# Optimization experiments

Hardware: AMD Instinct MI355X
Metric: run time of the kernel (lower is better)

## Reference

```python
import jax, jax.numpy as jnp
import numpy as np

N_NODES = 50000
N_EDGES = 800000
N_ENTS = 200000
N_RELS = 500
D = 128


def setup_inputs() -> dict:
    key = jax.random.key(0)
    ks = jax.random.split(key, 9)
    return {
        "prev_ent_embs": jax.random.normal(ks[0], (N_ENTS, D), dtype=jnp.float32),
        "rel_embs": jax.random.normal(ks[1], (N_RELS, D), dtype=jnp.float32),
        "loop_weight": jax.random.normal(ks[2], (D, D), dtype=jnp.float32) * 0.1,
        "evolve_loop_weight": jax.random.normal(ks[3], (D, D), dtype=jnp.float32) * 0.1,
        "weight_neighbor": jax.random.normal(ks[4], (D, D), dtype=jnp.float32) * 0.1,
        "node_id": jax.random.randint(ks[5], (N_NODES,), 0, N_ENTS, dtype=jnp.int64) if jax.config.jax_enable_x64 else jax.random.randint(ks[5], (N_NODES,), 0, N_ENTS, dtype=jnp.int32),
        "src": jax.random.randint(ks[6], (N_EDGES,), 0, N_NODES, dtype=jnp.int32),
        "dst": jax.random.randint(ks[7], (N_EDGES,), 0, N_NODES, dtype=jnp.int32),
        "etype": jax.random.randint(ks[8], (N_EDGES,), 0, N_RELS, dtype=jnp.int32),
    }


def reference(prev_ent_embs, rel_embs, loop_weight, evolve_loop_weight,
              weight_neighbor, node_id, src, dst, etype):
    n_nodes = node_id.shape[0]
    # node features gathered from global entity table
    h = prev_ent_embs[node_id]                                    # [N, D]

    # per-edge message: (h[src] + rel[type]) @ W_neighbor
    msg = (h[src] + rel_embs[etype]) @ weight_neighbor            # [E, D]

    # scatter-sum into destination nodes
    agg = jax.ops.segment_sum(msg, dst, num_segments=n_nodes)     # [N, D]

    # in-degree and norm (apply_func: h * in_norm, standard 1/in_degree)
    deg = jax.ops.segment_sum(jnp.ones_like(dst, dtype=h.dtype), dst,
                              num_segments=n_nodes)               # [N]
    has_in = deg > 0
    in_norm = jnp.where(has_in, 1.0 / jnp.maximum(deg, 1.0), 0.0)[:, None]
    agg = agg * in_norm

    # self-loop: loop_weight where in_degree>0, evolve_loop_weight otherwise
    loop_msg = jnp.where(has_in[:, None], h @ loop_weight, h @ evolve_loop_weight)

    # activation (dropout=0 -> identity in eval)
    return jax.nn.relu(agg + loop_msg)
```

## Files before the change

kernel.cpp:

```cpp
#include <hip/hip_runtime.h>
#include <hip/hip_bf16.h>
#include <stdint.h>

#define N_NODES 50000
#define N_EDGES 800000
#define N_ENTS  200000
#define N_RELS  500
#define DIM     128

#define DEGS 32
#define CAP  64

#define ZERO_REC ((int)(50000u | (500u << 16)))

using f32x4  = __attribute__((ext_vector_type(4))) float;
using bf16x8 = __attribute__((ext_vector_type(8))) short;

static __device__ __forceinline__ ushort f_to_bf16(float f) {
    __hip_bfloat16 h = __float2bfloat16(f);
    return *reinterpret_cast<ushort*>(&h);
}
static __device__ __forceinline__ uint pack2(float a, float b) {
    return (uint)f_to_bf16(a) | ((uint)f_to_bf16(b) << 16);
}
static __device__ __forceinline__ float blo(uint u) { return __uint_as_float(u << 16); }
static __device__ __forceinline__ float bhi(uint u) { return __uint_as_float(u & 0xffff0000u); }

__global__ __launch_bounds__(256) void k_front(
        const float* __restrict__ prev, const int* __restrict__ node_id,
        ushort* __restrict__ afull,
        const int* __restrict__ dst, const int* __restrict__ src,
        const int* __restrict__ etype,
        int* __restrict__ deg, uint* __restrict__ srcpk,
        const float* __restrict__ rel, ushort* __restrict__ rel_bf,
        const float* __restrict__ Wn, const float* __restrict__ Wl,
        ushort* __restrict__ WfT) {
    int blk = blockIdx.x;
    if (blk < 3125) {
        int e = blk * 256 + threadIdx.x;
        if (e < N_EDGES) {
            int dn = dst[e];
            uint rec = (uint)src[e] | ((uint)etype[e] << 16);
            int r = atomicAdd(&deg[dn * DEGS], 1);
            if (r < CAP) srcpk[dn * CAP + r] = rec;
        }
    } else if (blk < 6250) {
        int i = (blk - 3125) * 256 + threadIdx.x;
        int row = i >> 4, c = (i & 15) * 8;
        int nid = node_id[row];
        const float* p = prev + (size_t)nid * DIM + c;
        float4 v0 = *(const float4*)p;
        float4 v1 = *(const float4*)(p + 4);
        uint4 w;
        w.x = pack2(v0.x, v0.y);
        w.y = pack2(v0.z, v0.w);
        w.z = pack2(v1.x, v1.y);
        w.w = pack2(v1.z, v1.w);
        *(uint4*)(afull + (size_t)row * 256 + 128 + c) = w;
    } else if (blk < 6504) {
        int i = (blk - 6250) * 256 + threadIdx.x;
        if (i < 128 * 256) {
            int n = i >> 8, k = i & 255;
            float v = (k < 128) ? Wn[k * 128 + n] : Wl[(k - 128) * 128 + n];
            WfT[i] = f_to_bf16(v);
        } else {
            int j = i - 128 * 256;
            if (j < N_RELS * 64) {
                float2 v = *(const float2*)(rel + j * 2);
                *(uint*)(rel_bf + j * 2) = pack2(v.x, v.y);
            }
        }
    } else {
        int t = threadIdx.x;
        if (t < 128)       ((uint*)(afull + (size_t)50000 * 256))[t] = 0u;
        else if (t < 192)  ((uint*)(rel_bf + 500 * 128))[t - 128]    = 0u;
    }
}

__global__ __launch_bounds__(256) void k_agg(ushort* __restrict__ afull,
                                             const ushort* __restrict__ rel_bf,
                                             const uint* __restrict__ srcpk,
                                             const int* __restrict__ deg) {
    int wave = threadIdx.x >> 6, lane = threadIdx.x & 63;
    int n = blockIdx.x * 4 + wave;
    if (n >= N_NODES) return;
    int d = deg[n * DEGS];
    int cnt = min(d, CAP);
    int g = lane >> 4, q = lane & 15;
    const ushort* hb = afull + 128 + q * 8;
    const ushort* rb = rel_bf + q * 8;
    float acc[8] = {0.f, 0.f, 0.f, 0.f, 0.f, 0.f, 0.f, 0.f};

#define ACC4(hv, rv)                                              \
    acc[0] += blo(hv.x) + blo(rv.x); acc[1] += bhi(hv.x) + bhi(rv.x); \
    acc[2] += blo(hv.y) + blo(rv.y); acc[3] += bhi(hv.y) + bhi(rv.y); \
    acc[4] += blo(hv.z) + blo(rv.z); acc[5] += bhi(hv.z) + bhi(rv.z); \
    acc[6] += blo(hv.w) + blo(rv.w); acc[7] += bhi(hv.w) + bhi(rv.w);

    int rec = (lane < cnt) ? (int)srcpk[n * CAP + lane] : ZERO_REC;
    for (int j = 0; j < cnt; j += 8) {
        uint e0 = (uint)__shfl(rec, j + g);
        uint e1 = (uint)__shfl(rec, j + 4 + g);
        uint4 h0 = *(const uint4*)(hb + (size_t)(e0 & 0xffffu) * 256);
        uint4 r0 = *(const uint4*)(rb + (e0 >> 16) * 128);
        uint4 h1 = *(const uint4*)(hb + (size_t)(e1 & 0xffffu) * 256);
        uint4 r1 = *(const uint4*)(rb + (e1 >> 16) * 128);
        ACC4(h0, r0);
        ACC4(h1, r1);
    }
#undef ACC4

#pragma unroll
    for (int i = 0; i < 8; i++) {
        acc[i] += __shfl_xor(acc[i], 16);
        acc[i] += __shfl_xor(acc[i], 32);
    }
    float norm = (d > 0) ? 1.0f / (float)d : 0.0f;
    if (g == 0) {
        uint4 w;
        w.x = pack2(acc[0] * norm, acc[1] * norm);
        w.y = pack2(acc[2] * norm, acc[3] * norm);
        w.z = pack2(acc[4] * norm, acc[5] * norm);
        w.w = pack2(acc[6] * norm, acc[7] * norm);
        *(uint4*)(afull + (size_t)n * 256 + q * 8) = w;
    }
}

#define LDSK 264
__global__ __launch_bounds__(256) void k_mm(const ushort* __restrict__ afull,
                                            const ushort* __restrict__ WfT,
                                            float* __restrict__ out) {
    __shared__ ushort wl[128 * LDSK];
    for (int idx = threadIdx.x; idx < 128 * 32; idx += 256) {
        int n = idx >> 5, p = idx & 31;
        uint4 v = *(const uint4*)(WfT + n * 256 + p * 8);
        *(uint4*)(&wl[n * LDSK + p * 8]) = v;
    }
    __syncthreads();

    int wave = threadIdx.x >> 6, lane = threadIdx.x & 63;
    int m = lane & 15, quad = lane >> 4;
    int rowBase = blockIdx.x * 128 + wave * 32;

    f32x4 acc[2][8];
#pragma unroll
    for (int rt = 0; rt < 2; rt++)
#pragma unroll
        for (int ct = 0; ct < 8; ct++) acc[rt][ct] = f32x4{0.f, 0.f, 0.f, 0.f};

    int r0 = rowBase + m;      if (r0 > N_NODES - 1) r0 = N_NODES - 1;
    int r1 = rowBase + 16 + m; if (r1 > N_NODES - 1) r1 = N_NODES - 1;
    const ushort* pa0 = afull + (size_t)r0 * 256 + quad * 8;
    const ushort* pa1 = afull + (size_t)r1 * 256 + quad * 8;

#pragma unroll
    for (int ks = 0; ks < 8; ks++) {
        bf16x8 a0 = *(const bf16x8*)(pa0 + ks * 32);
        bf16x8 a1 = *(const bf16x8*)(pa1 + ks * 32);
#pragma unroll
        for (int ct = 0; ct < 8; ct++) {
            bf16x8 b = *(const bf16x8*)(&wl[(ct * 16 + m) * LDSK + ks * 32 + quad * 8]);
            acc[0][ct] = __builtin_amdgcn_mfma_f32_16x16x32_bf16(a0, b, acc[0][ct], 0, 0, 0);
            acc[1][ct] = __builtin_amdgcn_mfma_f32_16x16x32_bf16(a1, b, acc[1][ct], 0, 0, 0);
        }
    }

#pragma unroll
    for (int rt = 0; rt < 2; rt++) {
        int rbase = rowBase + rt * 16 + quad * 4;
#pragma unroll
        for (int reg = 0; reg < 4; reg++) {
            int grow = rbase + reg;
            if (grow < N_NODES) {
#pragma unroll
                for (int ct = 0; ct < 8; ct++) {
                    float v = acc[rt][ct][reg];
                    out[(size_t)grow * 128 + ct * 16 + m] = v > 0.f ? v : 0.f;
                }
            }
        }
    }
}

__global__ __launch_bounds__(256) void k_fixup(const ushort* __restrict__ afull,
                                               const float* __restrict__ We,
                                               const int* __restrict__ deg,
                                               float* __restrict__ out) {
    int n = blockIdx.x * 256 + threadIdx.x;
    if (n >= N_NODES) return;
    if (deg[n * DEGS] != 0) return;
    for (int c = 0; c < 128; c++) {
        float a = 0.f;
        for (int k = 0; k < 128; k++) {
            float h = blo((uint)afull[(size_t)n * 256 + 128 + k]);
            a += h * We[k * 128 + c];
        }
        out[(size_t)n * 128 + c] = a > 0.f ? a : 0.f;
    }
}

extern "C" void kernel_launch(void* const* d_in, const int* in_sizes, int n_in,
                              void* d_out, int out_size, void* d_ws, size_t ws_size,
                              hipStream_t stream) {
    const float* prev  = (const float*)d_in[0];
    const float* rel   = (const float*)d_in[1];
    const float* Wl    = (const float*)d_in[2];
    const float* We    = (const float*)d_in[3];
    const float* Wn    = (const float*)d_in[4];
    const int* node_id = (const int*)d_in[5];
    const int* src     = (const int*)d_in[6];
    const int* dst     = (const int*)d_in[7];
    const int* etype   = (const int*)d_in[8];
    float* out = (float*)d_out;

    char* ws = (char*)d_ws;
    ushort* afull  = (ushort*)(ws);
    ushort* WfT    = (ushort*)(ws + 25600512);
    ushort* rel_bf = (ushort*)(ws + 25666048);
    int* deg       = (int*)(ws + 25794304);
    uint* srcpk    = (uint*)(ws + 32194304);

    hipMemsetAsync(deg, 0, 6400000, stream);
    k_front <<<6505,  256, 0, stream>>>(prev, node_id, afull, dst, src, etype,
                                        deg, srcpk, rel, rel_bf, Wn, Wl, WfT);
    k_agg   <<<12500, 256, 0, stream>>>(afull, rel_bf, srcpk, deg);
    k_mm    <<<391,   256, 0, stream>>>(afull, WfT, out);
    k_fixup <<<196,   256, 0, stream>>>(afull, We, deg, out);
}
```

Baseline: 243.3 us.

## Vectorize edge bucketing, unroll aggregation gathers, fold zero-degree fixup into GEMM

Each thread in the edge-bucketing phase now handles four edges, loaded as int4 vectors, which cuts the front kernel's block count. The aggregation loop gathers 16 edges per iteration instead of 8 to keep more loads in flight. The separate fixup kernel for zero in-degree nodes is removed. Its scalar evolve-weight matmul now runs inside the GEMM epilogue behind a rarely taken branch, saving one launch at the cost of possible divergence inside the MFMA kernel.

New measurement: 270.0 us. 11.0% more time.

```diff
diff --git a/kernel.cpp b/kernel.cpp
--- a/kernel.cpp
+++ b/kernel.cpp
@@ -36,16 +36,25 @@
         const float* __restrict__ Wn, const float* __restrict__ Wl,
         ushort* __restrict__ WfT) {
     int blk = blockIdx.x;
-    if (blk < 3125) {
-        int e = blk * 256 + threadIdx.x;
+    if (blk < 782) {
+        int t = blk * 256 + threadIdx.x;
+        int e = t * 4;
         if (e < N_EDGES) {
-            int dn = dst[e];
-            uint rec = (uint)src[e] | ((uint)etype[e] << 16);
-            int r = atomicAdd(&deg[dn * DEGS], 1);
-            if (r < CAP) srcpk[dn * CAP + r] = rec;
-        }
-    } else if (blk < 6250) {
-        int i = (blk - 3125) * 256 + threadIdx.x;
+            int4 d4 = *(const int4*)(dst + e);
+            int4 s4 = *(const int4*)(src + e);
+            int4 t4 = *(const int4*)(etype + e);
+            int r;
+            r = atomicAdd(&deg[d4.x * DEGS], 1);
+            if (r < CAP) srcpk[d4.x * CAP + r] = (uint)s4.x | ((uint)t4.x << 16);
+            r = atomicAdd(&deg[d4.y * DEGS], 1);
+            if (r < CAP) srcpk[d4.y * CAP + r] = (uint)s4.y | ((uint)t4.y << 16);
+            r = atomicAdd(&deg[d4.z * DEGS], 1);
+            if (r < CAP) srcpk[d4.z * CAP + r] = (uint)s4.z | ((uint)t4.z << 16);
+            r = atomicAdd(&deg[d4.w * DEGS], 1);
+            if (r < CAP) srcpk[d4.w * CAP + r] = (uint)s4.w | ((uint)t4.w << 16);
+        }
+    } else if (blk < 3907) {
+        int i = (blk - 782) * 256 + threadIdx.x;
         int row = i >> 4, c = (i & 15) * 8;
         int nid = node_id[row];
         const float* p = prev + (size_t)nid * DIM + c;
@@ -57,8 +66,8 @@
         w.z = pack2(v1.x, v1.y);
         w.w = pack2(v1.z, v1.w);
         *(uint4*)(afull + (size_t)row * 256 + 128 + c) = w;
-    } else if (blk < 6504) {
-        int i = (blk - 6250) * 256 + threadIdx.x;
+    } else if (blk < 4161) {
+        int i = (blk - 3907) * 256 + threadIdx.x;
         if (i < 128 * 256) {
             int n = i >> 8, k = i & 255;
             float v = (k < 128) ? Wn[k * 128 + n] : Wl[(k - 128) * 128 + n];
@@ -98,15 +107,23 @@
     acc[6] += blo(hv.w) + blo(rv.w); acc[7] += bhi(hv.w) + bhi(rv.w);
 
     int rec = (lane < cnt) ? (int)srcpk[n * CAP + lane] : ZERO_REC;
-    for (int j = 0; j < cnt; j += 8) {
+    for (int j = 0; j < cnt; j += 16) {
         uint e0 = (uint)__shfl(rec, j + g);
         uint e1 = (uint)__shfl(rec, j + 4 + g);
+        uint e2 = (uint)__shfl(rec, j + 8 + g);
+        uint e3 = (uint)__shfl(rec, j + 12 + g);
         uint4 h0 = *(const uint4*)(hb + (size_t)(e0 & 0xffffu) * 256);
         uint4 r0 = *(const uint4*)(rb + (e0 >> 16) * 128);
         uint4 h1 = *(const uint4*)(hb + (size_t)(e1 & 0xffffu) * 256);
         uint4 r1 = *(const uint4*)(rb + (e1 >> 16) * 128);
+        uint4 h2 = *(const uint4*)(hb + (size_t)(e2 & 0xffffu) * 256);
+        uint4 r2 = *(const uint4*)(rb + (e2 >> 16) * 128);
+        uint4 h3 = *(const uint4*)(hb + (size_t)(e3 & 0xffffu) * 256);
+        uint4 r3 = *(const uint4*)(rb + (e3 >> 16) * 128);
         ACC4(h0, r0);
         ACC4(h1, r1);
+        ACC4(h2, r2);
+        ACC4(h3, r3);
     }
 #undef ACC4
 
@@ -129,6 +146,8 @@
 #define LDSK 264
 __global__ __launch_bounds__(256) void k_mm(const ushort* __restrict__ afull,
                                             const ushort* __restrict__ WfT,
+                                            const int* __restrict__ deg,
+                                            const float* __restrict__ We,
                                             float* __restrict__ out) {
     __shared__ ushort wl[128 * LDSK];
     for (int idx = threadIdx.x; idx < 128 * 32; idx += 256) {
@@ -172,30 +191,27 @@
         for (int reg = 0; reg < 4; reg++) {
             int grow = rbase + reg;
             if (grow < N_NODES) {
-#pragma unroll
-                for (int ct = 0; ct < 8; ct++) {
-                    float v = acc[rt][ct][reg];
-                    out[(size_t)grow * 128 + ct * 16 + m] = v > 0.f ? v : 0.f;
+                if (__builtin_expect(deg[grow * DEGS] == 0, 0)) {
+#pragma unroll 1
+                    for (int ct = 0; ct < 8; ct++) {
+                        int col = ct * 16 + m;
+                        float a = 0.f;
+#pragma unroll 1
+                        for (int k = 0; k < 128; k++) {
+                            float hv = blo((uint)afull[(size_t)grow * 256 + 128 + k]);
+                            a += hv * We[k * 128 + col];
+                        }
+                        out[(size_t)grow * 128 + col] = a > 0.f ? a : 0.f;
+                    }
+                } else {
+#pragma unroll
+                    for (int ct = 0; ct < 8; ct++) {
+                        float v = acc[rt][ct][reg];
+                        out[(size_t)grow * 128 + ct * 16 + m] = v > 0.f ? v : 0.f;
+                    }
                 }
             }
         }
-    }
-}
-
-__global__ __launch_bounds__(256) void k_fixup(const ushort* __restrict__ afull,
-                                               const float* __restrict__ We,
-                                               const int* __restrict__ deg,
-                                               float* __restrict__ out) {
-    int n = blockIdx.x * 256 + threadIdx.x;
-    if (n >= N_NODES) return;
-    if (deg[n * DEGS] != 0) return;
-    for (int c = 0; c < 128; c++) {
-        float a = 0.f;
-        for (int k = 0; k < 128; k++) {
-            float h = blo((uint)afull[(size_t)n * 256 + 128 + k]);
-            a += h * We[k * 128 + c];
-        }
-        out[(size_t)n * 128 + c] = a > 0.f ? a : 0.f;
     }
 }
 
@@ -221,9 +237,8 @@
     uint* srcpk    = (uint*)(ws + 32194304);
 
     hipMemsetAsync(deg, 0, 6400000, stream);
-    k_front <<<6505,  256, 0, stream>>>(prev, node_id, afull, dst, src, etype,
+    k_front <<<4162,  256, 0, stream>>>(prev, node_id, afull, dst, src, etype,
                                         deg, srcpk, rel, rel_bf, Wn, Wl, WfT);
     k_agg   <<<12500, 256, 0, stream>>>(afull, rel_bf, srcpk, deg);
-    k_mm    <<<391,   256, 0, stream>>>(afull, WfT, out);
-    k_fixup <<<196,   256, 0, stream>>>(afull, We, deg, out);
-}
+    k_mm    <<<391,   256, 0, stream>>>(afull, WfT, deg, We, out);
+}
```
